# Kernel tuning notes

Measured on AMD Instinct MI355X. Metric: run time of the kernel, lower is better.

## Reference

```python
import jax, jax.numpy as jnp
import numpy as np
import math

NH = 16
SIGMA = 1.5
KS = 7


def _gaussian_blur_16x16(x):
    # x: (N, 16, 16); torchvision GaussianBlur(7, 1.5) with reflect padding
    hx = jnp.arange(KS, dtype=x.dtype) - (KS - 1) / 2.0
    k1 = jnp.exp(-0.5 * (hx / SIGMA) ** 2)
    k1 = k1 / k1.sum()
    k2 = jnp.outer(k1, k1)[None, None]  # (1,1,7,7)
    pad = KS // 2
    xp = jnp.pad(x, ((0, 0), (pad, pad), (pad, pad)), mode='reflect')[:, None]
    y = jax.lax.conv_general_dilated(xp, k2, (1, 1), 'VALID')
    return y[:, 0]


def _normalize(w):
    mn, mx = w.min(), w.max()
    return (w - mn) / (mx - mn)


def _blurred_map(f, b_perm):
    # f, b_perm: (B, 256, 256)
    B = f.shape[0]
    bi = f * b_perm
    bi = bi.reshape(B * 256, 16, 16)
    bl = _gaussian_blur_16x16(bi)
    bl = jnp.clip(_normalize(bl), 0.0, 1.0)
    bl = bl.reshape(B, 256, 256)
    return bl * f * b_perm


def setup_inputs() -> dict:
    key = jax.random.key(0)
    ks = jax.random.split(key, 16)
    B, T, C = 4, 827, 1024
    inp = {
        'x': jax.random.normal(ks[0], (B, T, C), jnp.float32),
        'h': jax.random.normal(ks[1], (B, NH, 827, 827), jnp.float32) * 0.1,
        'f01': jax.random.uniform(ks[2], (B, 256, 256), jnp.float32),
        'f02': jax.random.uniform(ks[3], (B, 256, 256), jnp.float32),
        'f12': jax.random.uniform(ks[4], (B, 256, 256), jnp.float32),
        'b01': jax.random.uniform(ks[5], (B, 256, 256), jnp.float32),
        'b02': jax.random.uniform(ks[6], (B, 256, 256), jnp.float32),
        'b12': jax.random.uniform(ks[7], (B, 256, 256), jnp.float32),
        'Wq': jax.random.normal(ks[8], (C, C), jnp.float32) * 0.02,
        'bq': jnp.zeros((C,), jnp.float32),
        'Wk': jax.random.normal(ks[9], (C, C), jnp.float32) * 0.02,
        'bk': jnp.zeros((C,), jnp.float32),
        'Wv': jax.random.normal(ks[10], (C, C), jnp.float32) * 0.02,
        'bv': jnp.zeros((C,), jnp.float32),
        'Wp': jax.random.normal(ks[11], (C, C), jnp.float32) * 0.02,
        'bp': jnp.zeros((C,), jnp.float32),
    }
    return inp


def reference(x, h, f01, f02, f12, b01, b02, b12,
              Wq, bq, Wk, bk, Wv, bv, Wp, bp):
    B, T, C = x.shape
    hd = C // NH
    # QKV projections -> (B, NH, T, hd)
    def proj(W, b):
        return (x @ W + b).reshape(B, T, NH, hd).transpose(0, 2, 1, 3)
    q, k, v = proj(Wq, bq), proj(Wk, bk), proj(Wv, bv)

    att = jnp.einsum('bhtd,bhsd->bhts', q, k) * (1.0 / math.sqrt(hd))
    att = h[:, :, :T, :T] + att  # adaptive additive bias

    # bidirectional epipolar multiplicative masks with blur
    b01p = jnp.transpose(b01, (0, 2, 1))
    b02p = jnp.transpose(b02, (0, 2, 1))
    b12p = jnp.transpose(b12, (0, 2, 1))
    blur01 = _blurred_map(f01, b01p)[:, None]  # (B,1,256,256), broadcast over heads
    blur02 = _blurred_map(f02, b02p)[:, None]
    blur12 = _blurred_map(f12, b12p)[:, None]

    n1 = min(T - 285, 256)
    att = att.at[:, :, 285:285 + n1, 0:256].multiply(blur01[:, :, :n1])
    if T > 571:
        n2 = T - 571
        att = att.at[:, :, 571:T, 0:256].multiply(blur02[:, :, :n2])
        att = att.at[:, :, 571:T, 286:542].multiply(blur12[:, :, :n2])

    mask = jnp.tril(jnp.ones((T, T), dtype=bool))
    att = jnp.where(mask, att, -jnp.inf)
    att = jax.nn.softmax(att, axis=-1)

    y = jnp.einsum('bhts,bhsd->bhtd', att, v)
    y = y.transpose(0, 2, 1, 3).reshape(B, T, C)
    return y @ Wp + bp
```

## Files before the change

### kernel.cpp

```cpp
#include <hip/hip_runtime.h>
#include <math.h>

using bfrag8 = __attribute__((ext_vector_type(8))) short;
using facc4  = __attribute__((ext_vector_type(4))) float;

#define MFMA16(a,b,c) __builtin_amdgcn_mfma_f32_16x16x32_bf16((a),(b),(c),0,0,0)

#define T_SEQ 827
#define T_PAD 832
#define NHEAD 16
#define NEG_INF (-__builtin_inff())
#define CM_TOT 1179392

static __device__ __forceinline__ unsigned short f2bf(float f) {
    unsigned int x = __float_as_uint(f);
    unsigned int r = x + 0x7FFFu + ((x >> 16) & 1u);
    return (unsigned short)(r >> 16);
}

static __device__ __forceinline__ void gl16(const unsigned short* g, unsigned short* l) {
    __builtin_amdgcn_global_load_lds(
        (const __attribute__((address_space(1))) unsigned int*)g,
        (__attribute__((address_space(3))) unsigned int*)l,
        16, 0, 0);
}

__global__ __launch_bounds__(256) void k_front(const float* __restrict__ x,
                                               unsigned short* __restrict__ x_bf,
                                               float* __restrict__ cm,
                                               unsigned short* q, unsigned short* k,
                                               unsigned short* vT,
                                               const float* __restrict__ Wq,
                                               const float* __restrict__ Wk,
                                               const float* __restrict__ Wv,
                                               const float* __restrict__ Wp,
                                               unsigned short* __restrict__ Wt_out,
                                               const float* f01, const float* f02, const float* f12,
                                               const float* b01, const float* b02, const float* b12,
                                               float* __restrict__ bl,
                                               float* __restrict__ pmm) {
    __shared__ float tile[32][33];
    __shared__ float img[16][17], tmp[16][17];
    __shared__ float smn[4], smx[4];
    int bid = blockIdx.x, tid = threadIdx.x;

    if (bid < 3308) {
        int i = (bid * 256 + tid) * 4;
        float4 v = *reinterpret_cast<const float4*>(x + i);
        ushort4 o;
        o.x = f2bf(v.x); o.y = f2bf(v.y); o.z = f2bf(v.z); o.w = f2bf(v.w);
        *reinterpret_cast<ushort4*>(x_bf + i) = o;
    } else if (bid < 4460) {
        int base = (bid - 3308) * 1024 + tid * 4;
        if (base + 4 <= CM_TOT) {
            float4 one = {1.f, 1.f, 1.f, 1.f};
            *reinterpret_cast<float4*>(cm + base) = one;
        } else {
#pragma unroll
            for (int j = 0; j < 4; ++j)
                if (base + j < CM_TOT) cm[base + j] = 1.f;
        }
    } else if (bid < 4524) {
        int bh = bid - 4460;
        for (int i = tid; i < 320; i += 256) {
            int t = 827 + i / 64, d = i % 64;
            q[((size_t)bh * T_PAD + t) * 64 + d] = 0;
            k[((size_t)bh * T_PAD + t) * 64 + d] = 0;
        }
        for (int i = tid; i < 4096; i += 256) {
            int d = i >> 6, s = 768 + (i & 63);
            vT[((size_t)bh * 64 + d) * T_PAD + s] = 0;
        }
    } else if (bid < 8620) {
        int i = bid - 4524;
        int z = i >> 10, rem = i & 1023;
        int bx = rem & 31, by = rem >> 5;
        const float* W = (z == 0) ? Wq : (z == 1) ? Wk : (z == 2) ? Wv : Wp;
        unsigned short* Wt = Wt_out + (size_t)z * 1048576;
        int tx = tid & 31, ty0 = tid >> 5;
#pragma unroll
        for (int j = 0; j < 4; ++j) {
            int ty = ty0 + j * 8;
            tile[ty][tx] = W[(size_t)(by * 32 + ty) * 1024 + bx * 32 + tx];
        }
        __syncthreads();
#pragma unroll
        for (int j = 0; j < 4; ++j) {
            int ty = ty0 + j * 8;
            Wt[(size_t)(bx * 32 + ty) * 1024 + by * 32 + tx] = f2bf(tile[tx][ty]);
        }
    } else {
        int i = bid - 8620;
        int m = i >> 10, rem = i & 1023, b = rem >> 8, r = rem & 255;
        const float* f  = (m == 0) ? f01 : (m == 1) ? f02 : f12;
        const float* bm = (m == 0) ? b01 : (m == 1) ? b02 : b12;
        int ii = tid >> 4, j = tid & 15;

        float k1[7]; float ks = 0.f;
#pragma unroll
        for (int d = 0; d < 7; ++d) { float hx = (float)d - 3.f; k1[d] = expf(-0.5f * hx * hx / 2.25f); ks += k1[d]; }
#pragma unroll
        for (int d = 0; d < 7; ++d) k1[d] /= ks;

        size_t idx = (size_t)b * 65536 + (size_t)r * 256 + tid;
        float bi = f[idx] * bm[(size_t)b * 65536 + (size_t)tid * 256 + r];
        img[ii][j] = bi;
        __syncthreads();
        float ha = 0.f;
#pragma unroll
        for (int d = 0; d < 7; ++d) { int p = j - 3 + d; p = p < 0 ? -p : (p > 15 ? 30 - p : p); ha += k1[d] * img[ii][p]; }
        tmp[ii][j] = ha;
        __syncthreads();
        float v = 0.f;
#pragma unroll
        for (int d = 0; d < 7; ++d) { int p = ii - 3 + d; p = p < 0 ? -p : (p > 15 ? 30 - p : p); v += k1[d] * tmp[p][j]; }
        bl[(size_t)m * 262144 + idx] = v;

        float mn = v, mx = v;
#pragma unroll
        for (int off = 32; off; off >>= 1) { mn = fminf(mn, __shfl_xor(mn, off)); mx = fmaxf(mx, __shfl_xor(mx, off)); }
        int wid = tid >> 6, lane = tid & 63;
        if (lane == 0) { smn[wid] = mn; smx[wid] = mx; }
        __syncthreads();
        if (tid == 0) {
            mn = fminf(fminf(smn[0], smn[1]), fminf(smn[2], smn[3]));
            mx = fmaxf(fmaxf(smx[0], smx[1]), fmaxf(smx[2], smx[3]));
            pmm[2 * i]     = mn;
            pmm[2 * i + 1] = mx;
        }
    }
}

__global__ __launch_bounds__(256) void k_gemm_qkv(const unsigned short* __restrict__ A,
                                              const unsigned short* __restrict__ Bt,
                                              const float* __restrict__ b0, const float* __restrict__ b1,
                                              const float* __restrict__ b2,
                                              unsigned short* __restrict__ qo, unsigned short* __restrict__ ko,
                                              unsigned short* __restrict__ vo, int M,
                                              const float* f01, const float* f02, const float* f12,
                                              const float* b01, const float* b02, const float* b12,
                                              const float* __restrict__ bl,
                                              const float* __restrict__ pmm,
                                              float* __restrict__ cm) {
    __shared__ unsigned short As[4096];
    __shared__ unsigned short Bs[4096];
    int bid = blockIdx.x, tid = threadIdx.x;

    if (bid >= 624) {
        int i = bid - 624;
        int m = i >> 10, rem = i & 1023, b = rem >> 8, r = rem & 255;
        float mn = __builtin_inff(), mx = 0.f;
        for (int kk = tid; kk < 1024; kk += 256) {
            int e = m * 1024 + kk;
            mn = fminf(mn, pmm[2 * e]);
            mx = fmaxf(mx, pmm[2 * e + 1]);
        }
#pragma unroll
        for (int off = 32; off; off >>= 1) { mn = fminf(mn, __shfl_xor(mn, off)); mx = fmaxf(mx, __shfl_xor(mx, off)); }
        float* fs = reinterpret_cast<float*>(As);
        int wid = tid >> 6, lane = tid & 63;
        if (lane == 0) { fs[wid] = mn; fs[4 + wid] = mx; }
        __syncthreads();
        mn = fminf(fminf(fs[0], fs[1]), fminf(fs[2], fs[3]));
        mx = fmaxf(fmaxf(fs[4], fs[5]), fmaxf(fs[6], fs[7]));

        const float* f  = (m == 0) ? f01 : (m == 1) ? f02 : f12;
        const float* bm = (m == 0) ? b01 : (m == 1) ? b02 : b12;
        size_t idx = (size_t)b * 65536 + (size_t)r * 256 + tid;
        float w = (bl[(size_t)m * 262144 + idx] - mn) / (mx - mn);
        w = fminf(fmaxf(w, 0.f), 1.f);
        float val = w * f[idx] * bm[(size_t)b * 65536 + (size_t)tid * 256 + r];
        int row = (m == 0) ? r : r + 286;
        int col = (m == 2) ? tid + 286 : tid;
        cm[((size_t)b * 542 + row) * 544 + col] = val;
        return;
    }

    int swz = (bid & 7) * 78 + (bid >> 3);
    int m0 = (swz % 26) * 128, n0 = (swz / 26) * 128;
    int wid = tid >> 6, lane = tid & 63;
    int g = lane >> 4, l15 = lane & 15;
    int wm = wid >> 1, wn = wid & 1;
    facc4 acc[4][4] = {};

    int ar0 = m0 + (tid >> 2); if (ar0 > M - 1) ar0 = M - 1;
    int ar1 = m0 + 64 + (tid >> 2); if (ar1 > M - 1) ar1 = M - 1;
    const unsigned short* Ap0 = A + (size_t)ar0 * 1024 + (tid & 3) * 8;
    const unsigned short* Ap1 = A + (size_t)ar1 * 1024 + (tid & 3) * 8;
    const unsigned short* Bp0 = Bt + (size_t)(n0 + (tid >> 2)) * 1024 + (tid & 3) * 8;
    const unsigned short* Bp1 = Bp0 + (size_t)64 * 1024;
    unsigned short* asw = As + (wid << 9);
    unsigned short* bsw = Bs + (wid << 9);

    for (int k0 = 0; k0 < 1024; k0 += 32) {
        if (k0) __syncthreads();
        gl16(Ap0 + k0, asw);
        gl16(Ap1 + k0, asw + 2048);
        gl16(Bp0 + k0, bsw);
        gl16(Bp1 + k0, bsw + 2048);
        __syncthreads();
        bfrag8 af[4], bf[4];
#pragma unroll
        for (int mi = 0; mi < 4; ++mi)
            af[mi] = *reinterpret_cast<const bfrag8*>(&As[(wm * 64 + mi * 16 + l15) * 32 + g * 8]);
#pragma unroll
        for (int ni = 0; ni < 4; ++ni)
            bf[ni] = *reinterpret_cast<const bfrag8*>(&Bs[(wn * 64 + ni * 16 + l15) * 32 + g * 8]);
#pragma unroll
        for (int mi = 0; mi < 4; ++mi)
#pragma unroll
            for (int ni = 0; ni < 4; ++ni)
                acc[mi][ni] = MFMA16(af[mi], bf[ni], acc[mi][ni]);
    }

    int which = n0 >> 10;
    const float* bb = (which == 0 ? b0 : (which == 1 ? b1 : b2));
#pragma unroll
    for (int mi = 0; mi < 4; ++mi)
#pragma unroll
        for (int ni = 0; ni < 4; ++ni)
#pragma unroll
            for (int r = 0; r < 4; ++r) {
                int row = m0 + wm * 64 + mi * 16 + g * 4 + r;
                if (row >= M) continue;
                int col = n0 + wn * 64 + ni * 16 + l15;
                float v = acc[mi][ni][r] + bb[col & 1023];
                int b = row / T_SEQ, t = row - b * T_SEQ;
                int cc = col & 1023;
                int hh = cc >> 6, d = cc & 63;
                size_t bh = (size_t)(b * NHEAD + hh);
                if (which == 0) {
                    qo[(bh * T_PAD + t) * 64 + d] = f2bf(v);
                } else if (which == 1) {
                    int du = (((d >> 3) ^ (t & 7)) << 3) | (d & 7);
                    ko[(bh * T_PAD + t) * 64 + du] = f2bf(v);
                } else {
                    int sl = t & 63;
                    int su = (((sl >> 3) ^ (d & 7)) << 3) | (t & 7);
                    vo[(bh * 64 + d) * T_PAD + (t - sl) + su] = f2bf(v);
                }
            }
}

__global__ __launch_bounds__(256) void k_proj64(const unsigned short* __restrict__ A,
                                                const unsigned short* __restrict__ Bt,
                                                const float* __restrict__ bias,
                                                float* __restrict__ out, int M) {
    __shared__ unsigned short As[2048];
    __shared__ unsigned short Bs[2048];
    int bid = blockIdx.x, tid = threadIdx.x;
    int swz = (bid & 7) * 104 + (bid >> 3);
    int m0 = (swz % 52) * 64, n0 = (swz / 52) * 64;
    int wid = tid >> 6, lane = tid & 63;
    int g = lane >> 4, l15 = lane & 15;
    int wm = wid >> 1, wn = wid & 1;
    facc4 acc[2][2] = {};

    int ar = m0 + (tid >> 2); if (ar > M - 1) ar = M - 1;
    const unsigned short* Ap = A + (size_t)ar * 1024 + (tid & 3) * 8;
    const unsigned short* Bp = Bt + (size_t)(n0 + (tid >> 2)) * 1024 + (tid & 3) * 8;
    unsigned short* asw = As + (wid << 9);
    unsigned short* bsw = Bs + (wid << 9);

    for (int k0 = 0; k0 < 1024; k0 += 32) {
        if (k0) __syncthreads();
        gl16(Ap + k0, asw);
        gl16(Bp + k0, bsw);
        __syncthreads();
        bfrag8 af[2], bf[2];
#pragma unroll
        for (int mi = 0; mi < 2; ++mi)
            af[mi] = *reinterpret_cast<const bfrag8*>(&As[(wm * 32 + mi * 16 + l15) * 32 + g * 8]);
#pragma unroll
        for (int ni = 0; ni < 2; ++ni)
            bf[ni] = *reinterpret_cast<const bfrag8*>(&Bs[(wn * 32 + ni * 16 + l15) * 32 + g * 8]);
#pragma unroll
        for (int mi = 0; mi < 2; ++mi)
#pragma unroll
            for (int ni = 0; ni < 2; ++ni)
                acc[mi][ni] = MFMA16(af[mi], bf[ni], acc[mi][ni]);
    }

#pragma unroll
    for (int mi = 0; mi < 2; ++mi)
#pragma unroll
        for (int ni = 0; ni < 2; ++ni)
#pragma unroll
            for (int r = 0; r < 4; ++r) {
                int row = m0 + wm * 32 + mi * 16 + g * 4 + r;
                if (row >= M) continue;
                int col = n0 + wn * 32 + ni * 16 + l15;
                out[(size_t)row * 1024 + col] = acc[mi][ni][r] + bias[col];
            }
}

__global__ __launch_bounds__(256) void k_attn(const unsigned short* __restrict__ qb,
                                              const unsigned short* __restrict__ kb,
                                              const unsigned short* __restrict__ vT,
                                              const float* __restrict__ h,
                                              const float* __restrict__ cm,
                                              unsigned short* __restrict__ y) {
    int blk0 = blockIdx.x;
    int blk = (blk0 & 7) * 104 + (blk0 >> 3);
    int bh = blk / 13;
    int qt = 12 - (blk % 13);
    int b = bh >> 4, hh = bh & 15;
    int tid = threadIdx.x, wid = tid >> 6, lane = tid & 63;
    int g = lane >> 4, l15 = lane & 15;
    int t0 = qt * 64 + wid * 16;
    int t = t0 + l15;
    int tcl = t > 826 ? 826 : t;
    int ntiles = qt + 1;

    __shared__ unsigned short Ks[2][4096];
    __shared__ unsigned short Vs[2][4096];
    __shared__ unsigned short Ps[4][1024];
    unsigned short* pw = &Ps[wid][0];

    const unsigned short* Kbase = kb + (size_t)bh * T_PAD * 64;
    const unsigned short* Vbase = vT + (size_t)bh * 64 * T_PAD;
    const float* hrow = h + (size_t)bh * T_SEQ * T_SEQ + (size_t)tcl * T_SEQ;
    int rt = t - 285; rt = rt < 0 ? 0 : (rt > 541 ? 541 : rt);
    const float* cmrow = cm + ((size_t)b * 542 + rt) * 544;
    bool tm = (t >= 285);

    size_t qrow = ((size_t)bh * T_PAD + t) * 64 + g * 8;
    bfrag8 aq0 = *reinterpret_cast<const bfrag8*>(qb + qrow);
    bfrag8 aq1 = *reinterpret_cast<const bfrag8*>(qb + qrow + 32);

    auto stage = [&](int s0, int buf) {
        const unsigned short* kt = Kbase + (size_t)s0 * 64;
        unsigned short* kd = &Ks[buf][0] + (wid << 9);
        gl16(kt + tid * 8, kd);
        gl16(kt + 2048 + tid * 8, kd + 2048);
        const unsigned short* vt = Vbase + s0;
        unsigned short* vd = &Vs[buf][0] + (wid << 9);
        gl16(vt + (size_t)(tid >> 3) * T_PAD + (tid & 7) * 8, vd);
        gl16(vt + (size_t)((tid >> 3) + 32) * T_PAD + (tid & 7) * 8, vd + 2048);
    };

    auto loadh = [&](int s0t, float* hv, float* mv) {
#pragma unroll
        for (int nt = 0; nt < 4; ++nt) {
            int sb = s0t + nt * 16 + 4 * g;
            float h4[4];
            if (sb + 3 <= tcl) {
                __builtin_memcpy(h4, hrow + sb, 16);
            } else {
#pragma unroll
                for (int j = 0; j < 4; ++j) {
                    float hx = 0.f;
                    if (sb + j <= tcl) hx = hrow[sb + j];
                    h4[j] = hx;
                }
            }
            float m4[4];
            if (tm && sb <= 540) {
                __builtin_memcpy(m4, cmrow + sb, 16);
            } else {
#pragma unroll
                for (int j = 0; j < 4; ++j) m4[j] = 1.f;
            }
#pragma unroll
            for (int j = 0; j < 4; ++j) { hv[nt * 4 + j] = h4[j]; mv[nt * 4 + j] = m4[j]; }
        }
    };

    float m_r = NEG_INF, l_r = 0.f;
    facc4 acc[4] = {};
    float hv[16], mv[16];
    loadh(0, hv, mv);
    stage(0, 0);

    for (int it = 0; it < ntiles; ++it) {
        int cur = it & 1, s0 = it * 64;
        bool more = (it + 1 < ntiles);
        bool diag = !more;
        __syncthreads();
        if (more) stage(s0 + 64, cur ^ 1);

        facc4 sf[4] = {};
        __builtin_amdgcn_s_setprio(1);
#pragma unroll
        for (int nt = 0; nt < 4; ++nt) {
            int row = nt * 16 + l15;
            const unsigned short* kp = &Ks[cur][row * 64];
            bfrag8 k0 = *reinterpret_cast<const bfrag8*>(kp + ((g ^ (row & 7)) << 3));
            bfrag8 k1 = *reinterpret_cast<const bfrag8*>(kp + (((4 + g) ^ (row & 7)) << 3));
            sf[nt] = MFMA16(k0, aq0, sf[nt]);
            sf[nt] = MFMA16(k1, aq1, sf[nt]);
        }
        __builtin_amdgcn_s_setprio(0);

        float vmax = NEG_INF;
#pragma unroll
        for (int nt = 0; nt < 4; ++nt)
#pragma unroll
            for (int r = 0; r < 4; ++r) {
                float val = fmaf(sf[nt][r], 0.125f, hv[nt * 4 + r]) * mv[nt * 4 + r];
                if (diag) {
                    int s = s0 + nt * 16 + 4 * g + r;
                    val = (s <= tcl) ? val : NEG_INF;
                }
                sf[nt][r] = val;
                vmax = fmaxf(vmax, val);
            }

        if (more) loadh(s0 + 64, hv, mv);

        vmax = fmaxf(vmax, __shfl_xor(vmax, 16));
        vmax = fmaxf(vmax, __shfl_xor(vmax, 32));

        bool noresc = __all(vmax <= m_r + 6.0f);
        float mnew = fmaxf(m_r, vmax);
        float mexp = noresc ? m_r : mnew;

        float ps = 0.f;
#pragma unroll
        for (int nt = 0; nt < 4; ++nt)
#pragma unroll
            for (int r = 0; r < 4; ++r) {
                float p = __expf(sf[nt][r] - mexp);
                sf[nt][r] = p;
                ps += p;
            }
        ps += __shfl_xor(ps, 16);
        ps += __shfl_xor(ps, 32);

#pragma unroll
        for (int nt = 0; nt < 4; ++nt) {
            unsigned u0, u1;
            asm("v_cvt_pk_bf16_f32 %0, %1, %2" : "=v"(u0) : "v"(sf[nt][0]), "v"(sf[nt][1]));
            asm("v_cvt_pk_bf16_f32 %0, %1, %2" : "=v"(u1) : "v"(sf[nt][2]), "v"(sf[nt][3]));
            int el = (l15 * 64 + nt * 16 + 4 * g) ^ ((l15 & 7) << 3);
            uint2 uu; uu.x = u0; uu.y = u1;
            *reinterpret_cast<uint2*>(&pw[el]) = uu;
        }

        if (!noresc) {
            float scale = __expf(m_r - mnew);
            l_r = l_r * scale + ps;
#pragma unroll
            for (int r = 0; r < 4; ++r) {
                float sc = __int_as_float(__builtin_amdgcn_ds_bpermute((4 * g + r) * 4, __float_as_int(scale)));
#pragma unroll
                for (int dt = 0; dt < 4; ++dt) acc[dt][r] *= sc;
            }
            m_r = mnew;
        } else {
            l_r += ps;
        }

        __builtin_amdgcn_s_setprio(1);
#pragma unroll
        for (int c2 = 0; c2 < 2; ++c2) {
            int ela = (l15 * 64 + c2 * 32 + 8 * g) ^ ((l15 & 7) << 3);
            bfrag8 ap = *reinterpret_cast<const bfrag8*>(&pw[ela]);
#pragma unroll
            for (int dt = 0; dt < 4; ++dt) {
                int row = dt * 16 + l15;
                bfrag8 vf = *reinterpret_cast<const bfrag8*>(&Vs[cur][row * 64 + (((c2 * 4 + g) ^ (row & 7)) << 3)]);
                acc[dt] = MFMA16(ap, vf, acc[dt]);
            }
        }
        __builtin_amdgcn_s_setprio(0);
    }

    float linv = 1.0f / l_r;
#pragma unroll
    for (int r = 0; r < 4; ++r) {
        float li = __int_as_float(__builtin_amdgcn_ds_bpermute((4 * g + r) * 4, __float_as_int(linv)));
        int tt = t0 + 4 * g + r;
        if (tt < T_SEQ) {
#pragma unroll
            for (int dt = 0; dt < 4; ++dt)
                y[((size_t)(b * T_SEQ) + tt) * 1024 + hh * 64 + dt * 16 + l15] = f2bf(acc[dt][r] * li);
        }
    }
}

extern "C" void kernel_launch(void* const* d_in, const int* in_sizes, int n_in,
                              void* d_out, int out_size, void* d_ws, size_t ws_size,
                              hipStream_t stream) {
    const float* x   = (const float*)d_in[0];
    const float* h   = (const float*)d_in[1];
    const float* f01 = (const float*)d_in[2];
    const float* f02 = (const float*)d_in[3];
    const float* f12 = (const float*)d_in[4];
    const float* b01 = (const float*)d_in[5];
    const float* b02 = (const float*)d_in[6];
    const float* b12 = (const float*)d_in[7];
    const float* Wq  = (const float*)d_in[8];
    const float* bq  = (const float*)d_in[9];
    const float* Wk  = (const float*)d_in[10];
    const float* bk  = (const float*)d_in[11];
    const float* Wv  = (const float*)d_in[12];
    const float* bv  = (const float*)d_in[13];
    const float* Wp  = (const float*)d_in[14];
    const float* bp  = (const float*)d_in[15];

    char* ws = (char*)d_ws;
    float* pmm    = (float*)(ws + 256);
    float* bl     = (float*)(ws + 256 + 24576);
    float* cmb    = (float*)(ws + 256 + 24576 + 3145728);
    unsigned short* x_bf  = (unsigned short*)(ws + 256 + 24576 + 3145728 + 4717568);
    unsigned short* WtQKV = x_bf + (size_t)3308 * 1024;
    unsigned short* WtP   = WtQKV + (size_t)3072 * 1024;
    unsigned short* q_bf  = WtP + (size_t)1024 * 1024;
    unsigned short* k_bf  = q_bf + (size_t)64 * T_PAD * 64;
    unsigned short* vTb   = k_bf + (size_t)64 * T_PAD * 64;
    unsigned short* y_bf  = vTb  + (size_t)64 * T_PAD * 64;

    k_front<<<11692, 256, 0, stream>>>(x, x_bf, cmb, q_bf, k_bf, vTb,
                                       Wq, Wk, Wv, Wp, WtQKV,
                                       f01, f02, f12, b01, b02, b12, bl, pmm);
    k_gemm_qkv<<<3696, 256, 0, stream>>>(x_bf, WtQKV, bq, bk, bv, q_bf, k_bf, vTb, 3308,
                                         f01, f02, f12, b01, b02, b12, bl, pmm, cmb);
    k_attn<<<832, 256, 0, stream>>>(q_bf, k_bf, vTb, h, cmb, y_bf);
    k_proj64<<<832, 256, 0, stream>>>(y_bf, WtP, bp, (float*)d_out, 3308);
}
```

Baseline: 135.3 us.

## Double-buffer QKV GEMM LDS tiles with async prefetch of next K slice

Doubles the A/B shared-memory tiles in the QKV projection GEMM and prefetches the next K-slice through global_load_lds while MFMAs run on the current buffer. Explicit vmcnt waits and barriers replace the two __syncthreads per iteration, and setprio raises wave priority around the MFMA block. This is meant to hide global-load latency behind compute, at the cost of twice the LDS, which may lower occupancy. The hand-placed waitcnt and barrier sequence is also easy to get wrong.

```diff
diff --git a/kernel.cpp b/kernel.cpp
--- a/kernel.cpp
+++ b/kernel.cpp
@@ -142,8 +142,8 @@
                                               const float* __restrict__ bl,
                                               const float* __restrict__ pmm,
                                               float* __restrict__ cm) {
-    __shared__ unsigned short As[4096];
-    __shared__ unsigned short Bs[4096];
+    __shared__ unsigned short As[2][4096];
+    __shared__ unsigned short Bs[2][4096];
     int bid = blockIdx.x, tid = threadIdx.x;
 
     if (bid >= 624) {
@@ -157,7 +157,7 @@
         }
 #pragma unroll
         for (int off = 32; off; off >>= 1) { mn = fminf(mn, __shfl_xor(mn, off)); mx = fmaxf(mx, __shfl_xor(mx, off)); }
-        float* fs = reinterpret_cast<float*>(As);
+        float* fs = reinterpret_cast<float*>(&As[0][0]);
         int wid = tid >> 6, lane = tid & 63;
         if (lane == 0) { fs[wid] = mn; fs[4 + wid] = mx; }
         __syncthreads();
@@ -189,28 +189,44 @@
     const unsigned short* Ap1 = A + (size_t)ar1 * 1024 + (tid & 3) * 8;
     const unsigned short* Bp0 = Bt + (size_t)(n0 + (tid >> 2)) * 1024 + (tid & 3) * 8;
     const unsigned short* Bp1 = Bp0 + (size_t)64 * 1024;
-    unsigned short* asw = As + (wid << 9);
-    unsigned short* bsw = Bs + (wid << 9);
-
-    for (int k0 = 0; k0 < 1024; k0 += 32) {
-        if (k0) __syncthreads();
-        gl16(Ap0 + k0, asw);
-        gl16(Ap1 + k0, asw + 2048);
-        gl16(Bp0 + k0, bsw);
-        gl16(Bp1 + k0, bsw + 2048);
-        __syncthreads();
+
+    auto stage = [&](int koff, int buf) {
+        gl16(Ap0 + koff, &As[buf][0] + (wid << 9));
+        gl16(Ap1 + koff, &As[buf][0] + (wid << 9) + 2048);
+        gl16(Bp0 + koff, &Bs[buf][0] + (wid << 9));
+        gl16(Bp1 + koff, &Bs[buf][0] + (wid << 9) + 2048);
+    };
+
+    stage(0, 0);
+    for (int k0 = 0; k0 < 32; ++k0) {
+        int cur = k0 & 1;
+        bool morek = (k0 + 1 < 32);
+        if (morek) {
+            stage((k0 + 1) * 32, cur ^ 1);
+            asm volatile("s_waitcnt vmcnt(4)" ::: "memory");
+        } else {
+            asm volatile("s_waitcnt vmcnt(0)" ::: "memory");
+        }
+        __builtin_amdgcn_s_barrier();
+        __builtin_amdgcn_sched_barrier(0);
+
         bfrag8 af[4], bf[4];
 #pragma unroll
         for (int mi = 0; mi < 4; ++mi)
-            af[mi] = *reinterpret_cast<const bfrag8*>(&As[(wm * 64 + mi * 16 + l15) * 32 + g * 8]);
+            af[mi] = *reinterpret_cast<const bfrag8*>(&As[cur][(wm * 64 + mi * 16 + l15) * 32 + g * 8]);
 #pragma unroll
         for (int ni = 0; ni < 4; ++ni)
-            bf[ni] = *reinterpret_cast<const bfrag8*>(&Bs[(wn * 64 + ni * 16 + l15) * 32 + g * 8]);
+            bf[ni] = *reinterpret_cast<const bfrag8*>(&Bs[cur][(wn * 64 + ni * 16 + l15) * 32 + g * 8]);
+        __builtin_amdgcn_s_setprio(1);
 #pragma unroll
         for (int mi = 0; mi < 4; ++mi)
 #pragma unroll
             for (int ni = 0; ni < 4; ++ni)
                 acc[mi][ni] = MFMA16(af[mi], bf[ni], acc[mi][ni]);
+        __builtin_amdgcn_s_setprio(0);
+
+        __builtin_amdgcn_sched_barrier(0);
+        if (morek) __builtin_amdgcn_s_barrier();
     }
 
     int which = n0 >> 10;
```

Measured after the change: 134.1 us. Within noise of the previous version (-0.9%).
